# Kernel tuning notes

Measured on AMD Instinct MI355X. Metric: run time of the kernel, lower is better.

Reference implementation:

```python
import jax, jax.numpy as jnp
import numpy as np

N_NODES = 50000
N_EDGES = 800000
IN_CH = 128
HID = 128
NUM_CLASSES = 10
NUM_GRAPHS = 64


def _linear_params(key, fan_in, fan_out):
    kw, kb = jax.random.split(key)
    s = 1.0 / np.sqrt(fan_in)
    W = jax.random.uniform(kw, (fan_in, fan_out), jnp.float32, -s, s)
    b = jax.random.uniform(kb, (fan_out,), jnp.float32, -s, s)
    return W, b


def setup_inputs() -> dict:
    key = jax.random.key(0)
    ks = jax.random.split(key, 16)
    x = jax.random.normal(ks[0], (N_NODES, IN_CH), jnp.float32)
    edge_index = jax.random.randint(ks[1], (2, N_EDGES), 0, N_NODES, jnp.int64)
    batch = jnp.sort(jax.random.randint(ks[2], (N_NODES,), 0, NUM_GRAPHS, jnp.int64))
    inp = {"x": x, "edge_index": edge_index, "batch": batch}
    # conv layer 1 (in -> hid)
    inp["Wk1"], inp["bk1"] = _linear_params(ks[3], IN_CH, HID)
    inp["Wq1"], inp["bq1"] = _linear_params(ks[4], IN_CH, HID)
    inp["Wv1"], inp["bv1"] = _linear_params(ks[5], IN_CH, HID)
    inp["Ws1"], inp["bs1"] = _linear_params(ks[6], IN_CH, HID)
    inp["b1"] = jnp.zeros((HID,), jnp.float32)
    # conv layer 2 (hid -> hid)
    inp["Wk2"], inp["bk2"] = _linear_params(ks[7], HID, HID)
    inp["Wq2"], inp["bq2"] = _linear_params(ks[8], HID, HID)
    inp["Wv2"], inp["bv2"] = _linear_params(ks[9], HID, HID)
    inp["Ws2"], inp["bs2"] = _linear_params(ks[10], HID, HID)
    inp["b2"] = jnp.zeros((HID,), jnp.float32)
    # final fc
    inp["fcW"], inp["fcb"] = _linear_params(ks[11], HID, NUM_CLASSES)
    return inp


def _res_gated_conv(x, src, dst, Wk, bk, Wq, bq, Wv, bv, Ws, bs, b):
    # k from target node i, q and v from source node j (PyG ResGatedGraphConv)
    k = x @ Wk + bk            # [N, H]
    q = x @ Wq + bq            # [N, H]
    v = x @ Wv + bv            # [N, H]
    gate = jax.nn.sigmoid(k[dst] + q[src])   # [E, H]
    msg = gate * v[src]                       # [E, H]
    agg = jax.ops.segment_sum(msg, dst, num_segments=x.shape[0])
    return agg + x @ Ws + bs + b


def _global_mean_pool(x, batch, num_graphs):
    sums = jax.ops.segment_sum(x, batch, num_segments=num_graphs)
    cnts = jax.ops.segment_sum(jnp.ones((x.shape[0],), x.dtype), batch, num_segments=num_graphs)
    return sums / jnp.maximum(cnts, 1.0)[:, None]


def reference(x, edge_index, batch,
              Wk1, bk1, Wq1, bq1, Wv1, bv1, Ws1, bs1, b1,
              Wk2, bk2, Wq2, bq2, Wv2, bv2, Ws2, bs2, b2,
              fcW, fcb):
    src, dst = edge_index[0], edge_index[1]
    h = _res_gated_conv(x, src, dst, Wk1, bk1, Wq1, bq1, Wv1, bv1, Ws1, bs1, b1)
    h = jax.nn.relu(h)
    h = _res_gated_conv(h, src, dst, Wk2, bk2, Wq2, bq2, Wv2, bv2, Ws2, bs2, b2)
    h = jax.nn.relu(h)
    g = _global_mean_pool(h, batch, NUM_GRAPHS)   # [NUM_GRAPHS, HID]
    return g @ fcW + fcb                           # [NUM_GRAPHS, NUM_CLASSES]
```

## Files before the change

### kernel.cpp

```cpp
#include <hip/hip_runtime.h>
#include <math.h>


typedef __attribute__((ext_vector_type(8))) short short8;
typedef __attribute__((ext_vector_type(4))) float floatx4;
typedef __attribute__((ext_vector_type(8))) unsigned short ushort8v;

#define LOG2E 1.4426950408889634f

__device__ __forceinline__ unsigned short f2b(float f) {
  unsigned int u = __builtin_bit_cast(unsigned int, f);
  u += 0x7fff + ((u >> 16) & 1);
  return (unsigned short)(u >> 16);
}
__device__ __forceinline__ float b2f(unsigned short u) {
  return __builtin_bit_cast(float, ((unsigned int)u) << 16);
}
__device__ __forceinline__ float blo(unsigned int u) {
  return __builtin_bit_cast(float, u << 16);
}
__device__ __forceinline__ float bhi(unsigned int u) {
  return __builtin_bit_cast(float, u & 0xffff0000u);
}


__global__ __launch_bounds__(256) void hist_kernel(const int* __restrict__ dst,
                                                   int* __restrict__ cnt, int E) {
  int e = blockIdx.x * 256 + threadIdx.x;
  if (e < E) atomicAdd(&cnt[dst[e]], 1);
}

__global__ __launch_bounds__(256) void scan1_kernel(const int* __restrict__ cnt,
                                                    int* __restrict__ tmp_excl,
                                                    int* __restrict__ bsum, int n) {
  __shared__ int s[256];
  int t = threadIdx.x;
  int base = blockIdx.x * 512;
  int i0 = base + 2 * t, i1 = i0 + 1;
  int a0 = (i0 < n) ? cnt[i0] : 0;
  int a1 = (i1 < n) ? cnt[i1] : 0;
  int sum = a0 + a1;
  s[t] = sum;
  __syncthreads();
  for (int off = 1; off < 256; off <<= 1) {
    int v = (t >= off) ? s[t - off] : 0;
    __syncthreads();
    s[t] += v;
    __syncthreads();
  }
  int excl = s[t] - sum;
  if (i0 < n) tmp_excl[i0] = excl;
  if (i1 < n) tmp_excl[i1] = excl + a0;
  if (t == 255) bsum[blockIdx.x] = s[255];
}

__global__ __launch_bounds__(256) void finalize_rp_kernel(const int* __restrict__ tmp_excl,
                                                          const int* __restrict__ bsum,
                                                          int* __restrict__ row_ptr,
                                                          int* __restrict__ cursor,
                                                          int n, int E, int nb) {
  __shared__ int s[128];
  int t = threadIdx.x;
  if (t < 128) s[t] = (t < nb) ? bsum[t] : 0;
  __syncthreads();
  for (int off = 1; off < 128; off <<= 1) {
    int v = (t < 128 && t >= off) ? s[t - off] : 0;
    __syncthreads();
    if (t < 128) s[t] += v;
    __syncthreads();
  }
  int chunk = blockIdx.x >> 1;
  int boff = (chunk == 0) ? 0 : s[chunk - 1];
  int i = blockIdx.x * 256 + t;
  if (i < n) {
    int v = tmp_excl[i] + boff;
    row_ptr[i] = v;
    cursor[i] = v;
  }
  if (i == 0) row_ptr[n] = E;
}

__global__ __launch_bounds__(256) void scatter_kernel(const int* __restrict__ src,
                                                      const int* __restrict__ dst,
                                                      int* __restrict__ cursor,
                                                      int* __restrict__ es, int E) {
  int e = blockIdx.x * 256 + threadIdx.x;
  if (e < E) {
    int i = dst[e];
    int p = atomicAdd(&cursor[i], 1);
    es[p] = src[e];
  }
}


__global__ __launch_bounds__(256) void prep_kernel(
    const float* __restrict__ X, unsigned short* __restrict__ Xb, int total4,
    const float* __restrict__ Wk1, const float* __restrict__ Wq1,
    const float* __restrict__ Wv1, const float* __restrict__ Ws1,
    const float* __restrict__ Wk2, const float* __restrict__ Wq2,
    const float* __restrict__ Wv2, const float* __restrict__ Ws2,
    unsigned short* __restrict__ WT,
    const float* __restrict__ bk1, const float* __restrict__ bq1,
    const float* __restrict__ bv1, const float* __restrict__ bs1,
    const float* __restrict__ b1,
    const float* __restrict__ bk2, const float* __restrict__ bq2,
    const float* __restrict__ bv2, const float* __restrict__ bs2,
    const float* __restrict__ b2,
    float* __restrict__ bcat,
    int* __restrict__ cnt, int ncnt4, int nconvb, int nzerob) {
  int b = blockIdx.x;
  if (b < nconvb) {
    int i = b * 256 + threadIdx.x;
    if (i < total4) {
      float4 v = ((const float4*)X)[i];
      ushort4 o;
      o.x = f2b(v.x); o.y = f2b(v.y); o.z = f2b(v.z); o.w = f2b(v.w);
      ((ushort4*)Xb)[i] = o;
    }
    return;
  }
  b -= nconvb;
  if (b < nzerob) {
    int i = b * 256 + threadIdx.x;
    if (i < ncnt4) ((int4*)cnt)[i] = make_int4(0, 0, 0, 0);
    return;
  }
  b -= nzerob;
  if (b < 512) {
    int idx = b * 256 + threadIdx.x;
    int layer = idx >> 16;
    int rem = idx & 0xFFFF;
    int mat = rem >> 14;
    int nk = rem & 0x3FFF;
    int nn = nk >> 7, kk = nk & 127;
    int sel = layer * 4 + mat;
    const float* W = (sel == 0) ? Wk1 : (sel == 1) ? Wq1 : (sel == 2) ? Wv1 :
                     (sel == 3) ? Ws1 : (sel == 4) ? Wk2 : (sel == 5) ? Wq2 :
                     (sel == 6) ? Wv2 : Ws2;
    WT[idx] = f2b(W[kk * 128 + nn]);
    return;
  }
  b -= 512;
  {
    int idx = b * 256 + threadIdx.x;
    if (idx >= 1024) return;
    int layer = idx >> 9;
    int rem = idx & 511;
    int mat = rem >> 7, c = rem & 127;
    int sel = layer * 4 + mat;
    const float* bb = (sel == 0) ? bk1 : (sel == 1) ? bq1 : (sel == 2) ? bv1 :
                      (sel == 3) ? bs1 : (sel == 4) ? bk2 : (sel == 5) ? bq2 :
                      (sel == 6) ? bv2 : bs2;
    float v = bb[c];
    if (mat == 3) v += (layer == 0) ? b1[c] : b2[c];
    bcat[idx] = v;
  }
}


__global__ __launch_bounds__(256) void gemm_mfma_kernel(
    const unsigned short* __restrict__ Xb,
    const unsigned short* __restrict__ WT,
    const float* __restrict__ bcat,
    unsigned short* __restrict__ Kb, unsigned short* __restrict__ Qb,
    unsigned short* __restrict__ Vb, float* __restrict__ S, int n) {
  __shared__ unsigned short aT[128 * 136];

  int t = threadIdx.x;
  int row0 = blockIdx.x * 128;
  int m = blockIdx.y;

#pragma unroll
  for (int i = 0; i < 8; ++i) {
    int c = i * 256 + t;
    int r = c >> 4, col16 = c & 15;
    int4 v = make_int4(0, 0, 0, 0);
    if (row0 + r < n) v = *(const int4*)&Xb[(size_t)(row0 + r) * 128 + col16 * 8];
    *(int4*)&aT[r * 136 + col16 * 8] = v;
  }
  __syncthreads();

  int lane = t & 63, wid = t >> 6;
  int wy = wid >> 1, wx = wid & 1;
  int l15 = lane & 15, lq = lane >> 4;

  const unsigned short* WTm = WT + (size_t)m * 16384;

  floatx4 acc[4][4];
#pragma unroll
  for (int mf = 0; mf < 4; ++mf)
#pragma unroll
    for (int nf = 0; nf < 4; ++nf) acc[mf][nf] = (floatx4)(0.0f);

#pragma unroll
  for (int ks = 0; ks < 4; ++ks) {
    int kof = ks * 32 + lq * 8;
    short8 a[4], b[4];
#pragma unroll
    for (int mf = 0; mf < 4; ++mf)
      a[mf] = *(const short8*)&aT[(wy * 64 + mf * 16 + l15) * 136 + kof];
#pragma unroll
    for (int nf = 0; nf < 4; ++nf)
      b[nf] = *(const short8*)&WTm[(size_t)(wx * 64 + nf * 16 + l15) * 128 + kof];
#pragma unroll
    for (int mf = 0; mf < 4; ++mf)
#pragma unroll
      for (int nf = 0; nf < 4; ++nf)
        acc[mf][nf] = __builtin_amdgcn_mfma_f32_16x16x32_bf16(a[mf], b[nf], acc[mf][nf], 0, 0, 0);
  }

  __syncthreads();
  float* estage = (float*)aT + (size_t)wid * 1088;

  const float* bias = bcat + m * 128;
  int r4 = lane >> 2, cq4 = lane & 3;
  int col = wx * 64 + cq4 * 16;
  float4 bv[4];
#pragma unroll
  for (int j = 0; j < 4; ++j) bv[j] = *(const float4*)&bias[col + j * 4];

  unsigned short* Ob = (m == 0) ? Kb : (m == 1) ? Qb : Vb;

#pragma unroll
  for (int mf = 0; mf < 4; ++mf) {
#pragma unroll
    for (int nf = 0; nf < 4; ++nf)
#pragma unroll
      for (int i = 0; i < 4; ++i)
        estage[(lq * 4 + i) * 68 + nf * 16 + l15] = acc[mf][nf][i];
    int grow = row0 + wy * 64 + mf * 16 + r4;
    if (grow < n) {
      float4 p[4];
#pragma unroll
      for (int j = 0; j < 4; ++j) {
        float4 e = *(const float4*)&estage[r4 * 68 + cq4 * 16 + j * 4];
        p[j].x = e.x + bv[j].x; p[j].y = e.y + bv[j].y;
        p[j].z = e.z + bv[j].z; p[j].w = e.w + bv[j].w;
      }
      if (m < 3) {
        ushort8v o0, o1;
        o0[0] = f2b(p[0].x); o0[1] = f2b(p[0].y); o0[2] = f2b(p[0].z); o0[3] = f2b(p[0].w);
        o0[4] = f2b(p[1].x); o0[5] = f2b(p[1].y); o0[6] = f2b(p[1].z); o0[7] = f2b(p[1].w);
        o1[0] = f2b(p[2].x); o1[1] = f2b(p[2].y); o1[2] = f2b(p[2].z); o1[3] = f2b(p[2].w);
        o1[4] = f2b(p[3].x); o1[5] = f2b(p[3].y); o1[6] = f2b(p[3].z); o1[7] = f2b(p[3].w);
        *(ushort8v*)&Ob[(size_t)grow * 128 + col] = o0;
        *(ushort8v*)&Ob[(size_t)grow * 128 + col + 8] = o1;
      } else {
#pragma unroll
        for (int j = 0; j < 4; ++j)
          *(float4*)&S[(size_t)grow * 128 + col + j * 4] = p[j];
      }
    }
  }
}


__global__ __launch_bounds__(256) void edge_agg_kernel(
    const unsigned short* __restrict__ Kb, const unsigned short* __restrict__ Qb,
    const unsigned short* __restrict__ Vb, const float* __restrict__ S,
    const int* __restrict__ row_ptr, const int* __restrict__ es,
    unsigned short* __restrict__ Hb, int n) {
  int wid = threadIdx.x >> 6;
  int lane = threadIdx.x & 63;
  int node = blockIdx.x * 4 + wid;
  if (node >= n) return;
  int slot = lane >> 3;
  int l8 = lane & 7;
  int chb = l8 * 16;

  uint4 k0 = *(const uint4*)&Kb[(size_t)node * 128 + chb];
  uint4 k1 = *(const uint4*)&Kb[(size_t)node * 128 + chb + 8];
  float kcn[16];
#pragma unroll
  for (int p = 0; p < 4; ++p) {
    unsigned int u0 = ((const unsigned int*)&k0)[p];
    unsigned int u1 = ((const unsigned int*)&k1)[p];
    kcn[2 * p]     = blo(u0) * (-LOG2E);
    kcn[2 * p + 1] = bhi(u0) * (-LOG2E);
    kcn[8 + 2 * p]     = blo(u1) * (-LOG2E);
    kcn[8 + 2 * p + 1] = bhi(u1) * (-LOG2E);
  }

  float acc[16];
#pragma unroll
  for (int i = 0; i < 16; ++i) acc[i] = 0.0f;

  int e0 = row_ptr[node], e1 = row_ptr[node + 1];
  int e = e0 + slot;
  int j = (e < e1) ? es[e] : -1;
  while (j >= 0) {
    int en = e + 8;
    int jn = (en < e1) ? es[en] : -1;
    uint4 q0 = *(const uint4*)&Qb[(size_t)j * 128 + chb];
    uint4 q1 = *(const uint4*)&Qb[(size_t)j * 128 + chb + 8];
    uint4 v0 = *(const uint4*)&Vb[(size_t)j * 128 + chb];
    uint4 v1 = *(const uint4*)&Vb[(size_t)j * 128 + chb + 8];
#pragma unroll
    for (int p = 0; p < 4; ++p) {
      unsigned int qu0 = ((const unsigned int*)&q0)[p];
      unsigned int qu1 = ((const unsigned int*)&q1)[p];
      unsigned int vu0 = ((const unsigned int*)&v0)[p];
      unsigned int vu1 = ((const unsigned int*)&v1)[p];
      {
        float ex = __builtin_amdgcn_exp2f(fmaf(blo(qu0), -LOG2E, kcn[2 * p]));
        acc[2 * p] = fmaf(blo(vu0), __builtin_amdgcn_rcpf(1.0f + ex), acc[2 * p]);
      }
      {
        float ex = __builtin_amdgcn_exp2f(fmaf(bhi(qu0), -LOG2E, kcn[2 * p + 1]));
        acc[2 * p + 1] = fmaf(bhi(vu0), __builtin_amdgcn_rcpf(1.0f + ex), acc[2 * p + 1]);
      }
      {
        float ex = __builtin_amdgcn_exp2f(fmaf(blo(qu1), -LOG2E, kcn[8 + 2 * p]));
        acc[8 + 2 * p] = fmaf(blo(vu1), __builtin_amdgcn_rcpf(1.0f + ex), acc[8 + 2 * p]);
      }
      {
        float ex = __builtin_amdgcn_exp2f(fmaf(bhi(qu1), -LOG2E, kcn[8 + 2 * p + 1]));
        acc[8 + 2 * p + 1] = fmaf(bhi(vu1), __builtin_amdgcn_rcpf(1.0f + ex), acc[8 + 2 * p + 1]);
      }
    }
    e = en; j = jn;
  }

#pragma unroll
  for (int i = 0; i < 16; ++i) {
    acc[i] += __shfl_xor(acc[i], 8);
    acc[i] += __shfl_xor(acc[i], 16);
    acc[i] += __shfl_xor(acc[i], 32);
  }

  if (slot == 0) {
    ushort8v o0, o1;
#pragma unroll
    for (int q = 0; q < 4; ++q) {
      float4 sv = *(const float4*)&S[(size_t)node * 128 + chb + q * 4];
      float r0 = fmaxf(acc[q * 4 + 0] + sv.x, 0.f);
      float r1 = fmaxf(acc[q * 4 + 1] + sv.y, 0.f);
      float r2 = fmaxf(acc[q * 4 + 2] + sv.z, 0.f);
      float r3 = fmaxf(acc[q * 4 + 3] + sv.w, 0.f);
      if (q < 2) {
        o0[q * 4 + 0] = f2b(r0); o0[q * 4 + 1] = f2b(r1);
        o0[q * 4 + 2] = f2b(r2); o0[q * 4 + 3] = f2b(r3);
      } else {
        o1[(q - 2) * 4 + 0] = f2b(r0); o1[(q - 2) * 4 + 1] = f2b(r1);
        o1[(q - 2) * 4 + 2] = f2b(r2); o1[(q - 2) * 4 + 3] = f2b(r3);
      }
    }
    *(ushort8v*)&Hb[(size_t)node * 128 + chb] = o0;
    *(ushort8v*)&Hb[(size_t)node * 128 + chb + 8] = o1;
  }
}


__device__ __forceinline__ int lb_batch(const int* __restrict__ batch, int n, int key) {
  int lo = 0, hi = n;
  while (lo < hi) {
    int mid = (lo + hi) >> 1;
    if (batch[mid] < key) lo = mid + 1; else hi = mid;
  }
  return lo;
}

__global__ __launch_bounds__(256) void pool_sum_kernel(const unsigned short* __restrict__ Hb,
                                                       const int* __restrict__ batch,
                                                       float* __restrict__ partial, int n) {
  __shared__ float red[8 * 128];
  int g = blockIdx.x >> 4;
  int slice = blockIdx.x & 15;
  int t = threadIdx.x;
  int grp = t >> 5;
  int cq = t & 31;
  int s = lb_batch(batch, n, g), e = lb_batch(batch, n, g + 1);
  int cnt = e - s;
  int per = (cnt + 15) >> 4;
  int ss = s + slice * per;
  int ee = ss + per; if (ee > e) ee = e;

  float4 acc = make_float4(0.f, 0.f, 0.f, 0.f);
  for (int nd = ss + grp; nd < ee; nd += 8) {
    uint2 u = *(const uint2*)&Hb[(size_t)nd * 128 + cq * 4];
    acc.x += blo(u.x); acc.y += bhi(u.x);
    acc.z += blo(u.y); acc.w += bhi(u.y);
  }
  *(float4*)&red[grp * 128 + cq * 4] = acc;
  __syncthreads();
  if (t < 128) {
    float tot = 0.f;
#pragma unroll
    for (int g8 = 0; g8 < 8; ++g8) tot += red[g8 * 128 + t];
    partial[(size_t)slice * 8192 + g * 128 + t] = tot;
  }
}

__global__ __launch_bounds__(128) void fc_kernel(const float* __restrict__ partial,
                                                 const int* __restrict__ batch,
                                                 const float* __restrict__ fcW,
                                                 const float* __restrict__ fcb,
                                                 float* __restrict__ out, int n) {
  __shared__ float p[128];
  int g = blockIdx.x;
  int t = threadIdx.x;
  int cnt = lb_batch(batch, n, g + 1) - lb_batch(batch, n, g);
  float inv = 1.0f / (float)((cnt > 0) ? cnt : 1);
  float tot = 0.f;
#pragma unroll
  for (int s = 0; s < 16; ++s) tot += partial[(size_t)s * 8192 + g * 128 + t];
  p[t] = tot * inv;
  __syncthreads();
  if (t < 10) {
    float s = fcb[t];
    for (int c = 0; c < 128; ++c) s += p[c] * fcW[c * 10 + t];
    out[g * 10 + t] = s;
  }
}


extern "C" void kernel_launch(void* const* d_in, const int* in_sizes, int n_in,
                              void* d_out, int out_size, void* d_ws, size_t ws_size,
                              hipStream_t stream) {
  const float* x   = (const float*)d_in[0];
  const int* eidx  = (const int*)d_in[1];
  const int* batch = (const int*)d_in[2];
  const float* Wk1 = (const float*)d_in[3];  const float* bk1 = (const float*)d_in[4];
  const float* Wq1 = (const float*)d_in[5];  const float* bq1 = (const float*)d_in[6];
  const float* Wv1 = (const float*)d_in[7];  const float* bv1 = (const float*)d_in[8];
  const float* Ws1 = (const float*)d_in[9];  const float* bs1 = (const float*)d_in[10];
  const float* b1  = (const float*)d_in[11];
  const float* Wk2 = (const float*)d_in[12]; const float* bk2 = (const float*)d_in[13];
  const float* Wq2 = (const float*)d_in[14]; const float* bq2 = (const float*)d_in[15];
  const float* Wv2 = (const float*)d_in[16]; const float* bv2 = (const float*)d_in[17];
  const float* Ws2 = (const float*)d_in[18]; const float* bs2 = (const float*)d_in[19];
  const float* b2  = (const float*)d_in[20];
  const float* fcW = (const float*)d_in[21]; const float* fcb = (const float*)d_in[22];
  float* out = (float*)d_out;

  const int N = in_sizes[0] / 128;
  const int E = in_sizes[1] / 2;
  const int* src = eidx;
  const int* dst = eidx + E;

  char* w = (char*)d_ws;
  size_t off = 0;
  auto carve = [&](size_t bytes) -> void* {
    void* p = w + off;
    off += (bytes + 255) & ~size_t(255);
    return p;
  };
  const size_t featB16 = (size_t)N * 128 * 2;
  const size_t featB32 = (size_t)N * 128 * 4;
  unsigned short* Xb = (unsigned short*)carve(featB16);
  unsigned short* Kb = (unsigned short*)carve(featB16);
  unsigned short* Qb = (unsigned short*)carve(featB16);
  unsigned short* Vb = (unsigned short*)carve(featB16);
  unsigned short* Hb = (unsigned short*)carve(featB16);
  float* S  = (float*)carve(featB32);
  unsigned short* WT = (unsigned short*)carve(2 * 4 * 128 * 128 * 2);
  float* bcat = (float*)carve(1024 * 4);
  int* cnt      = (int*)carve(((size_t)N + 4) * 4);
  int* row_ptr  = (int*)carve((size_t)(N + 1) * 4);
  int* cursor   = (int*)carve((size_t)N * 4);
  int* tmp_excl = (int*)carve((size_t)N * 4);
  int* bsum     = (int*)carve(256 * 4);
  int* es       = (int*)carve((size_t)E * 4);
  float* partial = (float*)carve((size_t)16 * 64 * 128 * 4);
  (void)ws_size; (void)n_in; (void)out_size;

  int nconvb = (N * 32 + 255) / 256;
  int ncnt4 = (N + 3) / 4;
  int nzerob = (ncnt4 + 255) / 256;
  prep_kernel<<<nconvb + nzerob + 512 + 4, 256, 0, stream>>>(
      x, Xb, N * 32,
      Wk1, Wq1, Wv1, Ws1, Wk2, Wq2, Wv2, Ws2, WT,
      bk1, bq1, bv1, bs1, b1, bk2, bq2, bv2, bs2, b2, bcat,
      cnt, ncnt4, nconvb, nzerob);

  int nb512 = (N + 511) / 512;
  hist_kernel<<<(E + 255) / 256, 256, 0, stream>>>(dst, cnt, E);
  scan1_kernel<<<nb512, 256, 0, stream>>>(cnt, tmp_excl, bsum, N);
  finalize_rp_kernel<<<(N + 255) / 256, 256, 0, stream>>>(tmp_excl, bsum, row_ptr,
                                                          cursor, N, E, nb512);
  scatter_kernel<<<(E + 255) / 256, 256, 0, stream>>>(src, dst, cursor, es, E);

  dim3 ggrid((N + 127) / 128, 4);

  gemm_mfma_kernel<<<ggrid, 256, 0, stream>>>(Xb, WT, bcat, Kb, Qb, Vb, S, N);
  edge_agg_kernel<<<(N + 3) / 4, 256, 0, stream>>>(Kb, Qb, Vb, S, row_ptr, es, Hb, N);

  gemm_mfma_kernel<<<ggrid, 256, 0, stream>>>(Hb, WT + 65536, bcat + 512,
                                              Kb, Qb, Vb, S, N);
  edge_agg_kernel<<<(N + 3) / 4, 256, 0, stream>>>(Kb, Qb, Vb, S, row_ptr, es, Hb, N);

  pool_sum_kernel<<<1024, 256, 0, stream>>>(Hb, batch, partial, N);
  fc_kernel<<<64, 128, 0, stream>>>(partial, batch, fcW, fcb, out, N);
}
```

Measured before the change: 423.8 us.

## Fuse mean-pool into second edge aggregation and restructure gemm and edge loops

The second edge aggregation now adds its ReLU output straight into a per-graph pool buffer with atomics, so the separate pool_sum kernel and the write and re-read of the final hidden features go away. The pool buffer is zeroed in the prep kernel. Each GEMM block now computes two weight matrices from one staged A tile, halving the grid in y so the input tile is loaded into shared memory less often. The edge kernel uses 16 lanes of 8 channels per edge with 4 edge slots and prefetches the next edge's Q/V rows to overlap gathers. The trade-off is heavy atomic contention on only 64x128 pool addresses and float-atomic ordering nondeterminism.

```diff
diff --git a/kernel.cpp b/kernel.cpp
--- a/kernel.cpp
+++ b/kernel.cpp
@@ -12,9 +12,6 @@
   unsigned int u = __builtin_bit_cast(unsigned int, f);
   u += 0x7fff + ((u >> 16) & 1);
   return (unsigned short)(u >> 16);
-}
-__device__ __forceinline__ float b2f(unsigned short u) {
-  return __builtin_bit_cast(float, ((unsigned int)u) << 16);
 }
 __device__ __forceinline__ float blo(unsigned int u) {
   return __builtin_bit_cast(float, u << 16);
@@ -107,7 +104,8 @@
     const float* __restrict__ bv2, const float* __restrict__ bs2,
     const float* __restrict__ b2,
     float* __restrict__ bcat,
-    int* __restrict__ cnt, int ncnt4, int nconvb, int nzerob) {
+    int* __restrict__ cnt, float* __restrict__ pool,
+    int ncnt4, int nconvb, int nzerob) {
   int b = blockIdx.x;
   if (b < nconvb) {
     int i = b * 256 + threadIdx.x;
@@ -126,6 +124,12 @@
     return;
   }
   b -= nzerob;
+  if (b == 0) {
+    for (int i = threadIdx.x; i < 2048; i += 256)
+      ((float4*)pool)[i] = make_float4(0.f, 0.f, 0.f, 0.f);
+    return;
+  }
+  b -= 1;
   if (b < 512) {
     int idx = b * 256 + threadIdx.x;
     int layer = idx >> 16;
@@ -165,10 +169,10 @@
     unsigned short* __restrict__ Kb, unsigned short* __restrict__ Qb,
     unsigned short* __restrict__ Vb, float* __restrict__ S, int n) {
   __shared__ unsigned short aT[128 * 136];
+  __shared__ float estage_all[4][16 * 68];
 
   int t = threadIdx.x;
   int row0 = blockIdx.x * 128;
-  int m = blockIdx.y;
 
 #pragma unroll
   for (int i = 0; i < 8; ++i) {
@@ -183,72 +187,74 @@
   int lane = t & 63, wid = t >> 6;
   int wy = wid >> 1, wx = wid & 1;
   int l15 = lane & 15, lq = lane >> 4;
-
-  const unsigned short* WTm = WT + (size_t)m * 16384;
-
-  floatx4 acc[4][4];
-#pragma unroll
-  for (int mf = 0; mf < 4; ++mf)
-#pragma unroll
-    for (int nf = 0; nf < 4; ++nf) acc[mf][nf] = (floatx4)(0.0f);
-
-#pragma unroll
-  for (int ks = 0; ks < 4; ++ks) {
-    int kof = ks * 32 + lq * 8;
-    short8 a[4], b[4];
-#pragma unroll
-    for (int mf = 0; mf < 4; ++mf)
-      a[mf] = *(const short8*)&aT[(wy * 64 + mf * 16 + l15) * 136 + kof];
-#pragma unroll
-    for (int nf = 0; nf < 4; ++nf)
-      b[nf] = *(const short8*)&WTm[(size_t)(wx * 64 + nf * 16 + l15) * 128 + kof];
-#pragma unroll
-    for (int mf = 0; mf < 4; ++mf)
-#pragma unroll
-      for (int nf = 0; nf < 4; ++nf)
-        acc[mf][nf] = __builtin_amdgcn_mfma_f32_16x16x32_bf16(a[mf], b[nf], acc[mf][nf], 0, 0, 0);
-  }
-
-  __syncthreads();
-  float* estage = (float*)aT + (size_t)wid * 1088;
-
-  const float* bias = bcat + m * 128;
   int r4 = lane >> 2, cq4 = lane & 3;
   int col = wx * 64 + cq4 * 16;
-  float4 bv[4];
-#pragma unroll
-  for (int j = 0; j < 4; ++j) bv[j] = *(const float4*)&bias[col + j * 4];
-
-  unsigned short* Ob = (m == 0) ? Kb : (m == 1) ? Qb : Vb;
-
-#pragma unroll
-  for (int mf = 0; mf < 4; ++mf) {
-#pragma unroll
-    for (int nf = 0; nf < 4; ++nf)
-#pragma unroll
-      for (int i = 0; i < 4; ++i)
-        estage[(lq * 4 + i) * 68 + nf * 16 + l15] = acc[mf][nf][i];
-    int grow = row0 + wy * 64 + mf * 16 + r4;
-    if (grow < n) {
-      float4 p[4];
-#pragma unroll
-      for (int j = 0; j < 4; ++j) {
-        float4 e = *(const float4*)&estage[r4 * 68 + cq4 * 16 + j * 4];
-        p[j].x = e.x + bv[j].x; p[j].y = e.y + bv[j].y;
-        p[j].z = e.z + bv[j].z; p[j].w = e.w + bv[j].w;
-      }
-      if (m < 3) {
-        ushort8v o0, o1;
-        o0[0] = f2b(p[0].x); o0[1] = f2b(p[0].y); o0[2] = f2b(p[0].z); o0[3] = f2b(p[0].w);
-        o0[4] = f2b(p[1].x); o0[5] = f2b(p[1].y); o0[6] = f2b(p[1].z); o0[7] = f2b(p[1].w);
-        o1[0] = f2b(p[2].x); o1[1] = f2b(p[2].y); o1[2] = f2b(p[2].z); o1[3] = f2b(p[2].w);
-        o1[4] = f2b(p[3].x); o1[5] = f2b(p[3].y); o1[6] = f2b(p[3].z); o1[7] = f2b(p[3].w);
-        *(ushort8v*)&Ob[(size_t)grow * 128 + col] = o0;
-        *(ushort8v*)&Ob[(size_t)grow * 128 + col + 8] = o1;
-      } else {
-#pragma unroll
-        for (int j = 0; j < 4; ++j)
-          *(float4*)&S[(size_t)grow * 128 + col + j * 4] = p[j];
+  float* estage = estage_all[wid];
+
+#pragma unroll
+  for (int mm = 0; mm < 2; ++mm) {
+    int m = blockIdx.y * 2 + mm;
+    const unsigned short* WTm = WT + (size_t)m * 16384;
+
+    floatx4 acc[4][4];
+#pragma unroll
+    for (int mf = 0; mf < 4; ++mf)
+#pragma unroll
+      for (int nf = 0; nf < 4; ++nf) acc[mf][nf] = (floatx4)(0.0f);
+
+#pragma unroll
+    for (int ks = 0; ks < 4; ++ks) {
+      int kof = ks * 32 + lq * 8;
+      short8 a[4], b[4];
+#pragma unroll
+      for (int mf = 0; mf < 4; ++mf)
+        a[mf] = *(const short8*)&aT[(wy * 64 + mf * 16 + l15) * 136 + kof];
+#pragma unroll
+      for (int nf = 0; nf < 4; ++nf)
+        b[nf] = *(const short8*)&WTm[(size_t)(wx * 64 + nf * 16 + l15) * 128 + kof];
+#pragma unroll
+      for (int mf = 0; mf < 4; ++mf)
+#pragma unroll
+        for (int nf = 0; nf < 4; ++nf)
+          acc[mf][nf] = __builtin_amdgcn_mfma_f32_16x16x32_bf16(a[mf], b[nf], acc[mf][nf], 0, 0, 0);
+    }
+
+    const float* bias = bcat + m * 128;
+    float4 bv[4];
+#pragma unroll
+    for (int j = 0; j < 4; ++j) bv[j] = *(const float4*)&bias[col + j * 4];
+
+    unsigned short* Ob = (m == 0) ? Kb : (m == 1) ? Qb : Vb;
+
+#pragma unroll
+    for (int mf = 0; mf < 4; ++mf) {
+#pragma unroll
+      for (int nf = 0; nf < 4; ++nf)
+#pragma unroll
+        for (int i = 0; i < 4; ++i)
+          estage[(lq * 4 + i) * 68 + nf * 16 + l15] = acc[mf][nf][i];
+      int grow = row0 + wy * 64 + mf * 16 + r4;
+      if (grow < n) {
+        float4 p[4];
+#pragma unroll
+        for (int j = 0; j < 4; ++j) {
+          float4 e = *(const float4*)&estage[r4 * 68 + cq4 * 16 + j * 4];
+          p[j].x = e.x + bv[j].x; p[j].y = e.y + bv[j].y;
+          p[j].z = e.z + bv[j].z; p[j].w = e.w + bv[j].w;
+        }
+        if (m < 3) {
+          ushort8v o0, o1;
+          o0[0] = f2b(p[0].x); o0[1] = f2b(p[0].y); o0[2] = f2b(p[0].z); o0[3] = f2b(p[0].w);
+          o0[4] = f2b(p[1].x); o0[5] = f2b(p[1].y); o0[6] = f2b(p[1].z); o0[7] = f2b(p[1].w);
+          o1[0] = f2b(p[2].x); o1[1] = f2b(p[2].y); o1[2] = f2b(p[2].z); o1[3] = f2b(p[2].w);
+          o1[4] = f2b(p[3].x); o1[5] = f2b(p[3].y); o1[6] = f2b(p[3].z); o1[7] = f2b(p[3].w);
+          *(ushort8v*)&Ob[(size_t)grow * 128 + col] = o0;
+          *(ushort8v*)&Ob[(size_t)grow * 128 + col + 8] = o1;
+        } else {
+#pragma unroll
+          for (int j = 0; j < 4; ++j)
+            *(float4*)&S[(size_t)grow * 128 + col + j * 4] = p[j];
+        }
       }
     }
   }
@@ -259,94 +265,86 @@
     const unsigned short* __restrict__ Kb, const unsigned short* __restrict__ Qb,
     const unsigned short* __restrict__ Vb, const float* __restrict__ S,
     const int* __restrict__ row_ptr, const int* __restrict__ es,
-    unsigned short* __restrict__ Hb, int n) {
+    unsigned short* __restrict__ Hb, float* __restrict__ pool,
+    const int* __restrict__ batch, int mode, int n) {
   int wid = threadIdx.x >> 6;
   int lane = threadIdx.x & 63;
   int node = blockIdx.x * 4 + wid;
   if (node >= n) return;
-  int slot = lane >> 3;
-  int l8 = lane & 7;
-  int chb = l8 * 16;
-
-  uint4 k0 = *(const uint4*)&Kb[(size_t)node * 128 + chb];
-  uint4 k1 = *(const uint4*)&Kb[(size_t)node * 128 + chb + 8];
-  float kcn[16];
+  int slot = lane >> 4;
+  int l16 = lane & 15;
+  int chb = l16 * 8;
+
+  uint4 kk = *(const uint4*)&Kb[(size_t)node * 128 + chb];
+  float kcn[8];
 #pragma unroll
   for (int p = 0; p < 4; ++p) {
-    unsigned int u0 = ((const unsigned int*)&k0)[p];
-    unsigned int u1 = ((const unsigned int*)&k1)[p];
-    kcn[2 * p]     = blo(u0) * (-LOG2E);
-    kcn[2 * p + 1] = bhi(u0) * (-LOG2E);
-    kcn[8 + 2 * p]     = blo(u1) * (-LOG2E);
-    kcn[8 + 2 * p + 1] = bhi(u1) * (-LOG2E);
-  }
-
-  float acc[16];
-#pragma unroll
-  for (int i = 0; i < 16; ++i) acc[i] = 0.0f;
+    unsigned int u = ((const unsigned int*)&kk)[p];
+    kcn[2 * p]     = blo(u) * (-LOG2E);
+    kcn[2 * p + 1] = bhi(u) * (-LOG2E);
+  }
+
+  float acc[8];
+#pragma unroll
+  for (int i = 0; i < 8; ++i) acc[i] = 0.0f;
 
   int e0 = row_ptr[node], e1 = row_ptr[node + 1];
   int e = e0 + slot;
-  int j = (e < e1) ? es[e] : -1;
+  int j  = (e < e1) ? es[e] : -1;
+  int jn = (e + 4 < e1) ? es[e + 4] : -1;
+  uint4 q8 = make_uint4(0, 0, 0, 0), v8 = make_uint4(0, 0, 0, 0);
+  if (j >= 0) {
+    q8 = *(const uint4*)&Qb[(size_t)j * 128 + chb];
+    v8 = *(const uint4*)&Vb[(size_t)j * 128 + chb];
+  }
   while (j >= 0) {
-    int en = e + 8;
-    int jn = (en < e1) ? es[en] : -1;
-    uint4 q0 = *(const uint4*)&Qb[(size_t)j * 128 + chb];
-    uint4 q1 = *(const uint4*)&Qb[(size_t)j * 128 + chb + 8];
-    uint4 v0 = *(const uint4*)&Vb[(size_t)j * 128 + chb];
-    uint4 v1 = *(const uint4*)&Vb[(size_t)j * 128 + chb + 8];
+    uint4 q8n = make_uint4(0, 0, 0, 0), v8n = make_uint4(0, 0, 0, 0);
+    if (jn >= 0) {
+      q8n = *(const uint4*)&Qb[(size_t)jn * 128 + chb];
+      v8n = *(const uint4*)&Vb[(size_t)jn * 128 + chb];
+    }
+    int jnn = (e + 8 < e1) ? es[e + 8] : -1;
 #pragma unroll
     for (int p = 0; p < 4; ++p) {
-      unsigned int qu0 = ((const unsigned int*)&q0)[p];
-      unsigned int qu1 = ((const unsigned int*)&q1)[p];
-      unsigned int vu0 = ((const unsigned int*)&v0)[p];
-      unsigned int vu1 = ((const unsigned int*)&v1)[p];
+      unsigned int qu = ((const unsigned int*)&q8)[p];
+      unsigned int vu = ((const unsigned int*)&v8)[p];
       {
-        float ex = __builtin_amdgcn_exp2f(fmaf(blo(qu0), -LOG2E, kcn[2 * p]));
-        acc[2 * p] = fmaf(blo(vu0), __builtin_amdgcn_rcpf(1.0f + ex), acc[2 * p]);
+        float ex = __builtin_amdgcn_exp2f(fmaf(blo(qu), -LOG2E, kcn[2 * p]));
+        acc[2 * p] = fmaf(blo(vu), __builtin_amdgcn_rcpf(1.0f + ex), acc[2 * p]);
       }
       {
-        float ex = __builtin_amdgcn_exp2f(fmaf(bhi(qu0), -LOG2E, kcn[2 * p + 1]));
-        acc[2 * p + 1] = fmaf(bhi(vu0), __builtin_amdgcn_rcpf(1.0f + ex), acc[2 * p + 1]);
+        float ex = __builtin_amdgcn_exp2f(fmaf(bhi(qu), -LOG2E, kcn[2 * p + 1]));
+        acc[2 * p + 1] = fmaf(bhi(vu), __builtin_amdgcn_rcpf(1.0f + ex), acc[2 * p + 1]);
       }
-      {
-        float ex = __builtin_amdgcn_exp2f(fmaf(blo(qu1), -LOG2E, kcn[8 + 2 * p]));
-        acc[8 + 2 * p] = fmaf(blo(vu1), __builtin_amdgcn_rcpf(1.0f + ex), acc[8 + 2 * p]);
-      }
-      {
-        float ex = __builtin_amdgcn_exp2f(fmaf(bhi(qu1), -LOG2E, kcn[8 + 2 * p + 1]));
-        acc[8 + 2 * p + 1] = fmaf(bhi(vu1), __builtin_amdgcn_rcpf(1.0f + ex), acc[8 + 2 * p + 1]);
-      }
-    }
-    e = en; j = jn;
-  }
-
-#pragma unroll
-  for (int i = 0; i < 16; ++i) {
-    acc[i] += __shfl_xor(acc[i], 8);
+    }
+    e += 4; j = jn; jn = jnn; q8 = q8n; v8 = v8n;
+  }
+
+#pragma unroll
+  for (int i = 0; i < 8; ++i) {
     acc[i] += __shfl_xor(acc[i], 16);
     acc[i] += __shfl_xor(acc[i], 32);
   }
 
   if (slot == 0) {
-    ushort8v o0, o1;
-#pragma unroll
-    for (int q = 0; q < 4; ++q) {
-      float4 sv = *(const float4*)&S[(size_t)node * 128 + chb + q * 4];
-      float r0 = fmaxf(acc[q * 4 + 0] + sv.x, 0.f);
-      float r1 = fmaxf(acc[q * 4 + 1] + sv.y, 0.f);
-      float r2 = fmaxf(acc[q * 4 + 2] + sv.z, 0.f);
-      float r3 = fmaxf(acc[q * 4 + 3] + sv.w, 0.f);
-      if (q < 2) {
-        o0[q * 4 + 0] = f2b(r0); o0[q * 4 + 1] = f2b(r1);
-        o0[q * 4 + 2] = f2b(r2); o0[q * 4 + 3] = f2b(r3);
-      } else {
-        o1[(q - 2) * 4 + 0] = f2b(r0); o1[(q - 2) * 4 + 1] = f2b(r1);
-        o1[(q - 2) * 4 + 2] = f2b(r2); o1[(q - 2) * 4 + 3] = f2b(r3);
-      }
-    }
-    *(ushort8v*)&Hb[(size_t)node * 128 + chb] = o0;
-    *(ushort8v*)&Hb[(size_t)node * 128 + chb + 8] = o1;
+    float4 s0 = *(const float4*)&S[(size_t)node * 128 + chb];
+    float4 s1 = *(const float4*)&S[(size_t)node * 128 + chb + 4];
+    float r[8];
+    r[0] = fmaxf(acc[0] + s0.x, 0.f); r[1] = fmaxf(acc[1] + s0.y, 0.f);
+    r[2] = fmaxf(acc[2] + s0.z, 0.f); r[3] = fmaxf(acc[3] + s0.w, 0.f);
+    r[4] = fmaxf(acc[4] + s1.x, 0.f); r[5] = fmaxf(acc[5] + s1.y, 0.f);
+    r[6] = fmaxf(acc[6] + s1.z, 0.f); r[7] = fmaxf(acc[7] + s1.w, 0.f);
+    if (mode == 0) {
+      ushort8v o;
+#pragma unroll
+      for (int i = 0; i < 8; ++i) o[i] = f2b(r[i]);
+      *(ushort8v*)&Hb[(size_t)node * 128 + chb] = o;
+    } else {
+      int g = batch[node];
+      float* pg = &pool[g * 128 + chb];
+#pragma unroll
+      for (int i = 0; i < 8; ++i) atomicAdd(&pg[i], r[i]);
+    }
   }
 }
 
@@ -360,38 +358,7 @@
   return lo;
 }
 
-__global__ __launch_bounds__(256) void pool_sum_kernel(const unsigned short* __restrict__ Hb,
-                                                       const int* __restrict__ batch,
-                                                       float* __restrict__ partial, int n) {
-  __shared__ float red[8 * 128];
-  int g = blockIdx.x >> 4;
-  int slice = blockIdx.x & 15;
-  int t = threadIdx.x;
-  int grp = t >> 5;
-  int cq = t & 31;
-  int s = lb_batch(batch, n, g), e = lb_batch(batch, n, g + 1);
-  int cnt = e - s;
-  int per = (cnt + 15) >> 4;
-  int ss = s + slice * per;
-  int ee = ss + per; if (ee > e) ee = e;
-
-  float4 acc = make_float4(0.f, 0.f, 0.f, 0.f);
-  for (int nd = ss + grp; nd < ee; nd += 8) {
-    uint2 u = *(const uint2*)&Hb[(size_t)nd * 128 + cq * 4];
-    acc.x += blo(u.x); acc.y += bhi(u.x);
-    acc.z += blo(u.y); acc.w += bhi(u.y);
-  }
-  *(float4*)&red[grp * 128 + cq * 4] = acc;
-  __syncthreads();
-  if (t < 128) {
-    float tot = 0.f;
-#pragma unroll
-    for (int g8 = 0; g8 < 8; ++g8) tot += red[g8 * 128 + t];
-    partial[(size_t)slice * 8192 + g * 128 + t] = tot;
-  }
-}
-
-__global__ __launch_bounds__(128) void fc_kernel(const float* __restrict__ partial,
+__global__ __launch_bounds__(128) void fc_kernel(const float* __restrict__ pool,
                                                  const int* __restrict__ batch,
                                                  const float* __restrict__ fcW,
                                                  const float* __restrict__ fcb,
@@ -401,10 +368,7 @@
   int t = threadIdx.x;
   int cnt = lb_batch(batch, n, g + 1) - lb_batch(batch, n, g);
   float inv = 1.0f / (float)((cnt > 0) ? cnt : 1);
-  float tot = 0.f;
-#pragma unroll
-  for (int s = 0; s < 16; ++s) tot += partial[(size_t)s * 8192 + g * 128 + t];
-  p[t] = tot * inv;
+  p[t] = pool[g * 128 + t] * inv;
   __syncthreads();
   if (t < 10) {
     float s = fcb[t];
@@ -461,17 +425,17 @@
   int* tmp_excl = (int*)carve((size_t)N * 4);
   int* bsum     = (int*)carve(256 * 4);
   int* es       = (int*)carve((size_t)E * 4);
-  float* partial = (float*)carve((size_t)16 * 64 * 128 * 4);
+  float* pool   = (float*)carve(64 * 128 * 4);
   (void)ws_size; (void)n_in; (void)out_size;
 
   int nconvb = (N * 32 + 255) / 256;
   int ncnt4 = (N + 3) / 4;
   int nzerob = (ncnt4 + 255) / 256;
-  prep_kernel<<<nconvb + nzerob + 512 + 4, 256, 0, stream>>>(
+  prep_kernel<<<nconvb + nzerob + 1 + 512 + 4, 256, 0, stream>>>(
       x, Xb, N * 32,
       Wk1, Wq1, Wv1, Ws1, Wk2, Wq2, Wv2, Ws2, WT,
       bk1, bq1, bv1, bs1, b1, bk2, bq2, bv2, bs2, b2, bcat,
-      cnt, ncnt4, nconvb, nzerob);
+      cnt, pool, ncnt4, nconvb, nzerob);
 
   int nb512 = (N + 511) / 512;
   hist_kernel<<<(E + 255) / 256, 256, 0, stream>>>(dst, cnt, E);
@@ -480,15 +444,16 @@
                                                           cursor, N, E, nb512);
   scatter_kernel<<<(E + 255) / 256, 256, 0, stream>>>(src, dst, cursor, es, E);
 
-  dim3 ggrid((N + 127) / 128, 4);
+  dim3 ggrid((N + 127) / 128, 2);
 
   gemm_mfma_kernel<<<ggrid, 256, 0, stream>>>(Xb, WT, bcat, Kb, Qb, Vb, S, N);
-  edge_agg_kernel<<<(N + 3) / 4, 256, 0, stream>>>(Kb, Qb, Vb, S, row_ptr, es, Hb, N);
+  edge_agg_kernel<<<(N + 3) / 4, 256, 0, stream>>>(Kb, Qb, Vb, S, row_ptr, es,
+                                                   Hb, pool, batch, 0, N);
 
   gemm_mfma_kernel<<<ggrid, 256, 0, stream>>>(Hb, WT + 65536, bcat + 512,
                                               Kb, Qb, Vb, S, N);
-  edge_agg_kernel<<<(N + 3) / 4, 256, 0, stream>>>(Kb, Qb, Vb, S, row_ptr, es, Hb, N);
-
-  pool_sum_kernel<<<1024, 256, 0, stream>>>(Hb, batch, partial, N);
-  fc_kernel<<<64, 128, 0, stream>>>(partial, batch, fcW, fcb, out, N);
-}
+  edge_agg_kernel<<<(N + 3) / 4, 256, 0, stream>>>(Kb, Qb, Vb, S, row_ptr, es,
+                                                   Hb, pool, batch, 1, N);
+
+  fc_kernel<<<64, 128, 0, stream>>>(pool, batch, fcW, fcb, out, N);
+}
```

Result: slower. 900.9 us (+112.6%).
